# Optimization experiments

Hardware: AMD Instinct MI355X
Metric: run time of the kernel (lower is better)

The kernel has to match this reference:

```python
import jax, jax.numpy as jnp
import numpy as np
import math

LEVELS = 10
T = 4096              # 2**log2_hashmap_size, log2=12
F = 2                 # n_features_per_level
NMIN, NMAX = 16, 320
HIDDEN = 512
OMEGA = 30.0
COOR_DIM = LEVELS * F + 2   # 22: hash feats + raw coords
_b = math.exp((math.log(NMAX) - math.log(NMIN)) / (LEVELS - 1))
RES = [int(math.floor(NMIN * _b ** l)) for l in range(LEVELS)]
PRIME_Y = np.uint32(2654435761)
MASK = np.uint32(T - 1)


def _hash2(xi, yi):
    # instant-NGP style spatial hash for 2D, uint32 wraparound arithmetic
    return (xi ^ (yi * PRIME_Y)) & MASK


def hash_encode(coords, table):
    # coords: [N,2] in [0,1); table: [LEVELS, T, F]
    feats = []
    for l in range(LEVELS):
        x = coords * RES[l]               # [N,2] continuous grid coords
        x0 = jnp.floor(x)
        w = x - x0                        # bilinear weights in [0,1)
        xi = x0.astype(jnp.uint32)
        x0i, y0i = xi[:, 0], xi[:, 1]
        x1i, y1i = x0i + np.uint32(1), y0i + np.uint32(1)
        tab = table[l]
        f00 = tab[_hash2(x0i, y0i)]       # [N,F] gathers
        f10 = tab[_hash2(x1i, y0i)]
        f01 = tab[_hash2(x0i, y1i)]
        f11 = tab[_hash2(x1i, y1i)]
        wx = w[:, 0:1]
        wy = w[:, 1:2]
        fx0 = f00 + (f10 - f00) * wx
        fx1 = f01 + (f11 - f01) * wx
        feats.append(fx0 + (fx1 - fx0) * wy)
    return jnp.concatenate(feats + [coords], axis=-1)  # [N, COOR_DIM]


def sine(x, w, b):
    # SineLayer.forward: sin(linear(x)); omega_0 is baked into first-layer init
    return jnp.sin(x @ w.T + b)


def _sine_init(key, out_f, in_f, is_first):
    kw, kb = jax.random.split(key)
    if is_first:
        lim = OMEGA / in_f
    else:
        lim = math.sqrt(6.0 / in_f) / OMEGA
    w = jax.random.uniform(kw, (out_f, in_f), jnp.float32, -lim, lim)
    blim = 1.0 / math.sqrt(in_f)
    b = jax.random.uniform(kb, (out_f,), jnp.float32, -blim, blim)
    return w, b


def setup_inputs() -> dict:
    key = jax.random.key(0)
    ks = jax.random.split(key, 8)
    N = 262144
    coords = jax.random.uniform(ks[0], (N, 2), jnp.float32)
    table = jax.random.uniform(ks[1], (LEVELS, T, F), jnp.float32, -1e-4, 1e-4)
    w1, b1 = _sine_init(ks[2], HIDDEN, COOR_DIM, True)
    w2, b2 = _sine_init(ks[3], HIDDEN, HIDDEN, False)
    ws1, bs1 = _sine_init(ks[4], HIDDEN, COOR_DIM + HIDDEN, False)
    ws2, bs2 = _sine_init(ks[5], HIDDEN, HIDDEN, False)
    wo, bo = _sine_init(ks[6], 2, HIDDEN, False)
    return {"coords": coords, "table": table,
            "w1": w1, "b1": b1, "w2": w2, "b2": b2,
            "ws1": ws1, "bs1": bs1, "ws2": ws2, "bs2": bs2,
            "wo": wo, "bo": bo}


def reference(coords, table, w1, b1, w2, b2, ws1, bs1, ws2, bs2, wo, bo):
    h0 = hash_encode(coords, table)            # [N,22]
    h1 = sine(sine(h0, w1, b1), w2, b2)        # first block (n_flayer=2)
    h2 = jnp.concatenate([h1, h0], axis=-1)    # skip connection [N,534]
    h2 = sine(sine(h2, ws1, bs1), ws2, bs2)    # second block (n_slayer=2)
    return sine(h2, wo, bo)                    # [N,2]
```

## Files before the change

### kernel.cpp

```cpp
#include <hip/hip_runtime.h>
#include <hip/hip_bf16.h>
#include <math.h>

#define MBLK    64
#define H0_OFF  65536
#define LDSB    (H0_OFF + 64*64)
#define INV2PI  0.15915494309189535f

#define OFF_W1  0
#define OFF_W2  16384
#define OFF_WS1 (16384+262144)
#define OFF_WS2 (278528+278528)
#define OFF_WO  (557056+262144)
#define NPACK   (819200+1024)

typedef __attribute__((ext_vector_type(8))) short bf16x8;
typedef __attribute__((ext_vector_type(4))) float f32x4;

struct ResArr { int r[10]; };

__device__ __forceinline__ unsigned short f2bf(float f) {
    unsigned u = __float_as_uint(f);
    u += 0x7FFFu + ((u >> 16) & 1u);
    return (unsigned short)(u >> 16);
}
__device__ __forceinline__ float bf2f(unsigned short h) {
    return __uint_as_float(((unsigned)h) << 16);
}
__device__ __forceinline__ float hwsin(float x) {
    float r;
    asm("v_sin_f32 %0, %1" : "=v"(r) : "v"(x));
    return r;
}
__device__ __forceinline__ unsigned pack_bf16_rne(float a, float b) {
    unsigned ua = __float_as_uint(a);
    unsigned ub = __float_as_uint(b);
    ua += 0x7FFFu + ((ua >> 16) & 1u);
    ub += 0x7FFFu + ((ub >> 16) & 1u);
    return __builtin_amdgcn_perm(ub, ua, 0x07060302u);
}

__global__ void pack_weights(const float* __restrict__ w1, const float* __restrict__ w2,
                             const float* __restrict__ ws1, const float* __restrict__ ws2,
                             const float* __restrict__ wo, unsigned short* __restrict__ out)
{
    int i = blockIdx.x * 256 + threadIdx.x;
    if (i >= NPACK) return;
    float v;
    if (i < OFF_WO) {
        int il, KC, K_src, K_valid;
        const float* src;
        if (i < OFF_W2)       { il = i;           KC = 1;  K_src = 22;  K_valid = 22;  src = w1;  }
        else if (i < OFF_WS1) { il = i - OFF_W2;  KC = 16; K_src = 512; K_valid = 512; src = w2;  }
        else if (i < OFF_WS2) { il = i - OFF_WS1; KC = 17; K_src = 534; K_valid = 534; src = ws1; }
        else                  { il = i - OFF_WS2; KC = 16; K_src = 512; K_valid = 512; src = ws2; }
        int blk  = il >> 9, idx = il & 511;
        int lane = idx >> 3, j = idx & 7;
        int nf   = blk & 3;
        int rest = blk >> 2;
        int c    = rest % KC;
        int nb   = rest / KC;
        int n = nb * 64 + nf * 16 + (lane & 15);
        int k = c * 32 + (lane >> 4) * 8 + j;
        v = (k < K_valid) ? src[n * K_src + k] : 0.f;
    } else {
        v = wo[i - OFF_WO];
    }
    out[i] = f2bf(v * INV2PI);
}

template<int KSTEPS, bool TAIL, bool PREBAR>
__device__ __forceinline__ void mlp_layer(char* sm, const unsigned short* __restrict__ Wl,
                                          const float* __restrict__ bias,
                                          int wid, int lane)
{
    constexpr int NC = KSTEPS + (TAIL ? 1 : 0);
    const int n0 = wid * 64;
    const int lm = lane & 15;
    const int lk = lane >> 4;
    const int xm = lm << 4;

    const unsigned short* wnb = Wl + (unsigned)(wid * NC) * 2048 + (lane << 3);

    f32x4 acc[4][4];
    #pragma unroll
    for (int i = 0; i < 4; ++i)
        #pragma unroll
        for (int j = 0; j < 4; ++j) { f32x4 z = {0.f,0.f,0.f,0.f}; acc[i][j] = z; }

    #pragma unroll 1
    for (int ks = 0; ks < KSTEPS; ++ks) {
        bf16x8 w[4], a[4];
        #pragma unroll
        for (int nf = 0; nf < 4; ++nf)
            w[nf] = *(const bf16x8*)(wnb + ((ks*4 + nf) << 9));
        #pragma unroll
        for (int mf = 0; mf < 4; ++mf)
            a[mf] = *(const bf16x8*)(sm + ((((mf*16 + lm) << 10) + ks*64 + lk*16) ^ xm));
        #pragma unroll
        for (int mf = 0; mf < 4; ++mf)
            #pragma unroll
            for (int nf = 0; nf < 4; ++nf)
                acc[mf][nf] = __builtin_amdgcn_mfma_f32_16x16x32_bf16(w[nf], a[mf], acc[mf][nf], 0, 0, 0);
    }
    if (TAIL) {
        bf16x8 w[4], a[4];
        #pragma unroll
        for (int nf = 0; nf < 4; ++nf)
            w[nf] = *(const bf16x8*)(wnb + ((KSTEPS*4 + nf) << 9));
        #pragma unroll
        for (int mf = 0; mf < 4; ++mf)
            a[mf] = *(const bf16x8*)(sm + H0_OFF + ((((mf*16 + lm) << 6) + lk*16) ^ ((lm & 7) << 4)));
        #pragma unroll
        for (int mf = 0; mf < 4; ++mf)
            #pragma unroll
            for (int nf = 0; nf < 4; ++nf)
                acc[mf][nf] = __builtin_amdgcn_mfma_f32_16x16x32_bf16(w[nf], a[mf], acc[mf][nf], 0, 0, 0);
    }

    if (PREBAR) __syncthreads();

    #pragma unroll
    for (int nf = 0; nf < 4; ++nf) {
        const float4 bv = *(const float4*)(bias + n0 + nf*16 + lk*4);
        const int colb = (n0 + nf*16 + lk*4) * 2;
        #pragma unroll
        for (int mf = 0; mf < 4; ++mf) {
            float s0 = hwsin(acc[mf][nf][0] + bv.x * INV2PI);
            float s1 = hwsin(acc[mf][nf][1] + bv.y * INV2PI);
            float s2 = hwsin(acc[mf][nf][2] + bv.z * INV2PI);
            float s3 = hwsin(acc[mf][nf][3] + bv.w * INV2PI);
            uint2 pk;
            pk.x = pack_bf16_rne(s0, s1);
            pk.y = pack_bf16_rne(s2, s3);
            int row = mf*16 + lm;
            *(uint2*)(sm + (((row << 10) + colb) ^ xm)) = pk;
        }
    }
    __syncthreads();
}

__global__ __launch_bounds__(512) __attribute__((amdgpu_waves_per_eu(4))) void siren_fused(
    const float* __restrict__ coords, const float* __restrict__ table,
    const float* __restrict__ b1, const float* __restrict__ b2,
    const float* __restrict__ bs1, const float* __restrict__ bs2,
    const float* __restrict__ bo,
    const unsigned short* __restrict__ Wp,
    float* __restrict__ outp,
    ResArr res)
{
    extern __shared__ char sm[];
    const int tid = threadIdx.x;
    const int pbase = blockIdx.x * MBLK;

    {
        int p  = tid & 63;
        int lg = tid >> 6;
        float2 cc = ((const float2*)coords)[pbase + p];
        #pragma unroll
        for (int li = 0; li < 2; ++li) {
            int l = lg + 8 * li;
            if (l < 10) {
                float R  = (float)res.r[l];
                float fx = cc.x * R, fy = cc.y * R;
                float x0 = floorf(fx), y0 = floorf(fy);
                float wx = fx - x0,  wy = fy - y0;
                unsigned xi = (unsigned)x0, yi = (unsigned)y0;
                unsigned yp  = yi * 2654435761u;
                unsigned yp1 = (yi + 1u) * 2654435761u;
                unsigned h00 = (xi        ^ yp ) & 4095u;
                unsigned h10 = ((xi + 1u) ^ yp ) & 4095u;
                unsigned h01 = (xi        ^ yp1) & 4095u;
                unsigned h11 = ((xi + 1u) ^ yp1) & 4095u;
                const float2* tl = (const float2*)(table + l * 8192);
                float2 f00 = tl[h00], f10 = tl[h10], f01 = tl[h01], f11 = tl[h11];
                float a0 = f00.x + (f10.x - f00.x) * wx;
                float a1 = f01.x + (f11.x - f01.x) * wx;
                float g0 = a0 + (a1 - a0) * wy;
                float c0 = f00.y + (f10.y - f00.y) * wx;
                float c1 = f01.y + (f11.y - f01.y) * wx;
                float g1 = c0 + (c1 - c0) * wy;
                unsigned pk = (unsigned)f2bf(g0) | ((unsigned)f2bf(g1) << 16);
                *(unsigned*)(sm + H0_OFF + (((p << 6) + 4*l) ^ ((p & 7) << 4))) = pk;
            }
        }
        if (lg == 2) {
            unsigned pk = (unsigned)f2bf(cc.x) | ((unsigned)f2bf(cc.y) << 16);
            *(unsigned*)(sm + H0_OFF + (((p << 6) + 40) ^ ((p & 7) << 4))) = pk;
        }
        if (lg == 3) {
            #pragma unroll
            for (int bb = 44; bb < 64; bb += 4)
                *(unsigned*)(sm + H0_OFF + (((p << 6) + bb) ^ ((p & 7) << 4))) = 0u;
        }
    }
    __syncthreads();

    const int wid  = tid >> 6;
    const int lane = tid & 63;

    mlp_layer<0,  true,  false>(sm, Wp + OFF_W1,  b1,  wid, lane);
    mlp_layer<16, false, true >(sm, Wp + OFF_W2,  b2,  wid, lane);
    mlp_layer<16, true,  true >(sm, Wp + OFF_WS1, bs1, wid, lane);
    mlp_layer<16, false, true >(sm, Wp + OFF_WS2, bs2, wid, lane);

    {
        int p = tid >> 3, g = tid & 7;
        const unsigned short* wo0 = Wp + OFF_WO + g * 64;
        const unsigned short* wo1 = wo0 + 512;
        int xm = (p & 15) << 4;
        float s0 = 0.f, s1 = 0.f;
        #pragma unroll
        for (int kk = 0; kk < 8; ++kk) {
            int off = ((p << 10) + g*128 + kk*16) ^ xm;
            bf16x8 av  = *(const bf16x8*)(sm + off);
            bf16x8 w0  = *(const bf16x8*)(wo0 + kk * 8);
            bf16x8 w1v = *(const bf16x8*)(wo1 + kk * 8);
            #pragma unroll
            for (int j = 0; j < 8; ++j) {
                float a = bf2f((unsigned short)av[j]);
                s0 += a * bf2f((unsigned short)w0[j]);
                s1 += a * bf2f((unsigned short)w1v[j]);
            }
        }
        #pragma unroll
        for (int m = 1; m < 8; m <<= 1) {
            s0 += __shfl_xor(s0, m, 64);
            s1 += __shfl_xor(s1, m, 64);
        }
        if (g == 0) {
            float2 o;
            o.x = hwsin(s0 + bo[0] * INV2PI);
            o.y = hwsin(s1 + bo[1] * INV2PI);
            ((float2*)outp)[pbase + p] = o;
        }
    }
}

extern "C" void kernel_launch(void* const* d_in, const int* in_sizes, int n_in,
                              void* d_out, int out_size, void* d_ws, size_t ws_size,
                              hipStream_t stream)
{
    const float* coords = (const float*)d_in[0];
    const float* table  = (const float*)d_in[1];
    const float* w1  = (const float*)d_in[2];
    const float* b1  = (const float*)d_in[3];
    const float* w2  = (const float*)d_in[4];
    const float* b2  = (const float*)d_in[5];
    const float* ws1 = (const float*)d_in[6];
    const float* bs1 = (const float*)d_in[7];
    const float* ws2 = (const float*)d_in[8];
    const float* bs2 = (const float*)d_in[9];
    const float* wo  = (const float*)d_in[10];
    const float* bo  = (const float*)d_in[11];

    unsigned short* Wp = (unsigned short*)d_ws;
    float* outp = (float*)d_out;

    ResArr res;
    double bb = exp((log(320.0) - log(16.0)) / 9.0);
    for (int l = 0; l < 10; ++l) res.r[l] = (int)floor(16.0 * pow(bb, (double)l));

    (void)hipFuncSetAttribute((const void*)siren_fused,
                              hipFuncAttributeMaxDynamicSharedMemorySize, LDSB);

    int N = in_sizes[0] / 2;

    pack_weights<<<(NPACK + 255) / 256, 256, 0, stream>>>(w1, w2, ws1, ws2, wo, Wp);
    siren_fused<<<N / MBLK, 512, LDSB, stream>>>(coords, table, b1, b2, bs1, bs2, bo,
                                                 Wp, outp, res);
}
```

Baseline: 405.3 us.

## Chunk LDS activations by K-step and compute output layer with MFMA

Activations in LDS are reorganized into 4 KB chunks, one per 32-wide K-step, each with a row-XOR swizzle. This makes A-operand addressing a simple pointer increment, and weight pointers now use scalar increments. The final 512->2 layer, previously scalar FMA dot products with shuffle reductions, now uses MFMA with weights zero-padded to 16 output columns, and the two K-halves are reduced through LDS. The cost is extra barriers and padded MFMA work in the output layer, plus a changed epilogue write pattern that could introduce bank conflicts.

```diff
diff --git a/kernel.cpp b/kernel.cpp
--- a/kernel.cpp
+++ b/kernel.cpp
@@ -3,8 +3,9 @@
 #include <math.h>
 
 #define MBLK    64
+#define CHUNK   4096
 #define H0_OFF  65536
-#define LDSB    (H0_OFF + 64*64)
+#define LDSB    (H0_OFF + CHUNK)
 #define INV2PI  0.15915494309189535f
 
 #define OFF_W1  0
@@ -12,7 +13,7 @@
 #define OFF_WS1 (16384+262144)
 #define OFF_WS2 (278528+278528)
 #define OFF_WO  (557056+262144)
-#define NPACK   (819200+1024)
+#define NPACK   (819200+8192)
 
 typedef __attribute__((ext_vector_type(8))) short bf16x8;
 typedef __attribute__((ext_vector_type(4))) float f32x4;
@@ -64,7 +65,11 @@
         int k = c * 32 + (lane >> 4) * 8 + j;
         v = (k < K_valid) ? src[n * K_src + k] : 0.f;
     } else {
-        v = wo[i - OFF_WO];
+        int j = i - OFF_WO;
+        int h = j >> 12, ks = (j >> 9) & 7, lane = (j >> 3) & 63, jj = j & 7;
+        int n = lane & 15;
+        int k = h * 256 + ks * 32 + (lane >> 4) * 8 + jj;
+        v = (n < 2) ? wo[n * 512 + k] : 0.f;
     }
     out[i] = f2bf(v * INV2PI);
 }
@@ -78,9 +83,11 @@
     const int n0 = wid * 64;
     const int lm = lane & 15;
     const int lk = lane >> 4;
-    const int xm = lm << 4;
-
-    const unsigned short* wnb = Wl + (unsigned)(wid * NC) * 2048 + (lane << 3);
+    const int sw = (lm & 7) << 4;
+    const int rbase = (lm*64 + lk*16) ^ sw;
+
+    const unsigned short* up = Wl + (unsigned)(__builtin_amdgcn_readfirstlane(wid) * NC) * 2048;
+    const int lo8 = lane << 3;
 
     f32x4 acc[4][4];
     #pragma unroll
@@ -88,29 +95,32 @@
         #pragma unroll
         for (int j = 0; j < 4; ++j) { f32x4 z = {0.f,0.f,0.f,0.f}; acc[i][j] = z; }
 
+    const char* ab = sm + rbase;
     #pragma unroll 1
     for (int ks = 0; ks < KSTEPS; ++ks) {
         bf16x8 w[4], a[4];
         #pragma unroll
         for (int nf = 0; nf < 4; ++nf)
-            w[nf] = *(const bf16x8*)(wnb + ((ks*4 + nf) << 9));
-        #pragma unroll
-        for (int mf = 0; mf < 4; ++mf)
-            a[mf] = *(const bf16x8*)(sm + ((((mf*16 + lm) << 10) + ks*64 + lk*16) ^ xm));
+            w[nf] = *(const bf16x8*)(up + nf*512 + lo8);
+        #pragma unroll
+        for (int mf = 0; mf < 4; ++mf)
+            a[mf] = *(const bf16x8*)(ab + mf*1024);
         #pragma unroll
         for (int mf = 0; mf < 4; ++mf)
             #pragma unroll
             for (int nf = 0; nf < 4; ++nf)
                 acc[mf][nf] = __builtin_amdgcn_mfma_f32_16x16x32_bf16(w[nf], a[mf], acc[mf][nf], 0, 0, 0);
+        up += 2048;
+        ab += CHUNK;
     }
     if (TAIL) {
         bf16x8 w[4], a[4];
         #pragma unroll
         for (int nf = 0; nf < 4; ++nf)
-            w[nf] = *(const bf16x8*)(wnb + ((KSTEPS*4 + nf) << 9));
-        #pragma unroll
-        for (int mf = 0; mf < 4; ++mf)
-            a[mf] = *(const bf16x8*)(sm + H0_OFF + ((((mf*16 + lm) << 6) + lk*16) ^ ((lm & 7) << 4)));
+            w[nf] = *(const bf16x8*)(up + nf*512 + lo8);
+        #pragma unroll
+        for (int mf = 0; mf < 4; ++mf)
+            a[mf] = *(const bf16x8*)(sm + H0_OFF + rbase + mf*1024);
         #pragma unroll
         for (int mf = 0; mf < 4; ++mf)
             #pragma unroll
@@ -120,21 +130,27 @@
 
     if (PREBAR) __syncthreads();
 
+    int R[4], C[4];
+    #pragma unroll
+    for (int mf = 0; mf < 4; ++mf)
+        R[mf] = ((mf*16 + lm) * 64) ^ (sw & 64);
+    #pragma unroll
+    for (int nf = 0; nf < 4; ++nf)
+        C[nf] = (((nf & 1)*32 + lk*8) ^ (sw & 48)) + (wid*2 + (nf >> 1)) * CHUNK;
+
     #pragma unroll
     for (int nf = 0; nf < 4; ++nf) {
         const float4 bv = *(const float4*)(bias + n0 + nf*16 + lk*4);
-        const int colb = (n0 + nf*16 + lk*4) * 2;
         #pragma unroll
         for (int mf = 0; mf < 4; ++mf) {
-            float s0 = hwsin(acc[mf][nf][0] + bv.x * INV2PI);
-            float s1 = hwsin(acc[mf][nf][1] + bv.y * INV2PI);
-            float s2 = hwsin(acc[mf][nf][2] + bv.z * INV2PI);
-            float s3 = hwsin(acc[mf][nf][3] + bv.w * INV2PI);
+            float s0 = hwsin(fmaf(bv.x, INV2PI, acc[mf][nf][0]));
+            float s1 = hwsin(fmaf(bv.y, INV2PI, acc[mf][nf][1]));
+            float s2 = hwsin(fmaf(bv.z, INV2PI, acc[mf][nf][2]));
+            float s3 = hwsin(fmaf(bv.w, INV2PI, acc[mf][nf][3]));
             uint2 pk;
             pk.x = pack_bf16_rne(s0, s1);
             pk.y = pack_bf16_rne(s2, s3);
-            int row = mf*16 + lm;
-            *(uint2*)(sm + (((row << 10) + colb) ^ xm)) = pk;
+            *(uint2*)(sm + (R[mf] + C[nf])) = pk;
         }
     }
     __syncthreads();
@@ -205,35 +221,35 @@
     mlp_layer<16, false, true >(sm, Wp + OFF_WS2, bs2, wid, lane);
 
     {
-        int p = tid >> 3, g = tid & 7;
-        const unsigned short* wo0 = Wp + OFF_WO + g * 64;
-        const unsigned short* wo1 = wo0 + 512;
-        int xm = (p & 15) << 4;
-        float s0 = 0.f, s1 = 0.f;
-        #pragma unroll
-        for (int kk = 0; kk < 8; ++kk) {
-            int off = ((p << 10) + g*128 + kk*16) ^ xm;
-            bf16x8 av  = *(const bf16x8*)(sm + off);
-            bf16x8 w0  = *(const bf16x8*)(wo0 + kk * 8);
-            bf16x8 w1v = *(const bf16x8*)(wo1 + kk * 8);
-            #pragma unroll
-            for (int j = 0; j < 8; ++j) {
-                float a = bf2f((unsigned short)av[j]);
-                s0 += a * bf2f((unsigned short)w0[j]);
-                s1 += a * bf2f((unsigned short)w1v[j]);
-            }
-        }
-        #pragma unroll
-        for (int m = 1; m < 8; m <<= 1) {
-            s0 += __shfl_xor(s0, m, 64);
-            s1 += __shfl_xor(s1, m, 64);
-        }
-        if (g == 0) {
-            float2 o;
-            o.x = hwsin(s0 + bo[0] * INV2PI);
-            o.y = hwsin(s1 + bo[1] * INV2PI);
-            ((float2*)outp)[pbase + p] = o;
-        }
+        const int lm = lane & 15;
+        const int lk = lane >> 4;
+        const int r0 = (wid & 3) * 16;
+        const int h  = __builtin_amdgcn_readfirstlane(wid) >> 2;
+        const int rbase = (((r0 + lm)*64 + lk*16) ^ ((lm & 7) << 4)) + h*8*CHUNK;
+        const unsigned short* uo = Wp + OFF_WO + h*4096;
+        const int lo8 = lane << 3;
+
+        f32x4 acc = {0.f, 0.f, 0.f, 0.f};
+        #pragma unroll
+        for (int ks = 0; ks < 8; ++ks) {
+            bf16x8 w = *(const bf16x8*)(uo + ks*512 + lo8);
+            bf16x8 a = *(const bf16x8*)(sm + rbase + ks*CHUNK);
+            acc = __builtin_amdgcn_mfma_f32_16x16x32_bf16(w, a, acc, 0, 0, 0);
+        }
+        __syncthreads();
+        if (lk == 0) {
+            float2 part; part.x = acc[0]; part.y = acc[1];
+            *(float2*)(sm + H0_OFF + (h*64 + r0 + lm)*8) = part;
+        }
+    }
+    __syncthreads();
+    if (tid < 64) {
+        float2 p0 = *(const float2*)(sm + H0_OFF + tid*8);
+        float2 p1 = *(const float2*)(sm + H0_OFF + 512 + tid*8);
+        float2 o;
+        o.x = hwsin(fmaf(bo[0], INV2PI, p0.x + p1.x));
+        o.y = hwsin(fmaf(bo[1], INV2PI, p0.y + p1.y));
+        ((float2*)outp)[pbase + tid] = o;
     }
 }
 
```

After: 373.0 us. -8.0%, faster.
